# Optimization experiments

Hardware: AMD Instinct MI355X
Metric: run time of the kernel (lower is better)

Reference implementation:

```python
import jax, jax.numpy as jnp
import numpy as np

B, D = 16384, 4096
H1, H2 = 64, 32
EPS_BN = 1e-5


def _lin(k, fi, fo):
    return 0.02 * jax.random.normal(k, (fi, fo), dtype=jnp.float32)


def setup_inputs() -> dict:
    key = jax.random.key(0)
    ks = jax.random.split(key, 8)
    x = jax.random.uniform(ks[0], (B, D), dtype=jnp.float32)
    return {
        "x": x,
        "W_in": _lin(ks[1], D, H1), "b_in": jnp.zeros((H1,), jnp.float32),
        "g1": jnp.ones((H1,), jnp.float32), "bt1": jnp.zeros((H1,), jnp.float32),
        "W_enc": _lin(ks[2], H1, H2), "b_enc": jnp.zeros((H2,), jnp.float32),
        "g2": jnp.ones((H2,), jnp.float32), "bt2": jnp.zeros((H2,), jnp.float32),
        "W_dec": _lin(ks[3], H2, H1), "b_dec": jnp.zeros((H1,), jnp.float32),
        "g3": jnp.ones((H1,), jnp.float32), "bt3": jnp.zeros((H1,), jnp.float32),
        "W_pi": _lin(ks[4], H1, D), "b_pi": jnp.zeros((D,), jnp.float32),
        "W_m": _lin(ks[5], H1, D), "b_m": jnp.zeros((D,), jnp.float32),
        "W_th": _lin(ks[6], H1, D), "b_th": jnp.zeros((D,), jnp.float32),
    }


def preprocess_data(data):
    # torch: s = data.sum(1); s /= median(s); norm = inverse(diag(s)) @ data + 1
    # inverse(diag(s)) @ data is exactly a per-row division by s.
    s = jnp.sum(data, axis=1)
    n = s.shape[0]
    med = jnp.sort(s)[(n - 1) // 2]  # torch.median = lower median
    s = s / med
    norm = jnp.log(data / s[:, None] + 1.0)
    # torch .std() is unbiased (ddof=1)
    return (norm - norm.mean()) / norm.std(ddof=1)


def batchnorm(h, gamma, beta):
    # training-mode BatchNorm1d: biased batch variance, eps=1e-5
    mu = h.mean(axis=0)
    var = h.var(axis=0)
    return (h - mu) * jax.lax.rsqrt(var + EPS_BN) * gamma + beta


def reference(x, W_in, b_in, g1, bt1, W_enc, b_enc, g2, bt2,
              W_dec, b_dec, g3, bt3, W_pi, b_pi, W_m, b_m, W_th, b_th):
    h = preprocess_data(x)
    h = jax.nn.relu(batchnorm(h @ W_in + b_in, g1, bt1))
    h = jax.nn.relu(batchnorm(h @ W_enc + b_enc, g2, bt2))
    h = jax.nn.relu(batchnorm(h @ W_dec + b_dec, g3, bt3))
    PI = jax.nn.sigmoid(h @ W_pi + b_pi)
    M = jnp.exp(h @ W_m + b_m)
    THETA = jnp.exp(h @ W_th + b_th)
    return (PI, M, THETA)
```

## Files before the change

### kernel.cpp

```cpp
#include <hip/hip_runtime.h>

#define BATCH 16384
#define DIM   4096

typedef __bf16 bf16x8 __attribute__((ext_vector_type(8)));
typedef float  f32x4  __attribute__((ext_vector_type(4)));
typedef unsigned short u16x8 __attribute__((ext_vector_type(8)));
typedef unsigned short u16x4 __attribute__((ext_vector_type(4)));

#define BAR_LGKM() asm volatile("s_waitcnt lgkmcnt(0)\ns_barrier" ::: "memory")

#define WS_ROWSUM 0
#define WS_MED    16384
#define WS_NPART  16400
#define WS_SC3    17536
#define WS_CC3    17600
#define WS_A2PART 18432
#define WS_A3PART 34816
#define WS_CPART  67584
#define WS_R      133120
#define WS_A2     1181696
#define WS_A3     1705984
#define WS_WTIN   2754560
#define WS_WTO    2885632

__device__ __forceinline__ unsigned short f2bf(float f){
  union { float f; unsigned u; } v; v.f = f;
  unsigned r = v.u + 0x7FFFu + ((v.u >> 16) & 1u);
  return (unsigned short)(r >> 16);
}

__global__ __launch_bounds__(256) void k_prep_rowsum(
    const float* __restrict__ x, const float* __restrict__ Win,
    const float* __restrict__ Wpi, const float* __restrict__ Wm,
    const float* __restrict__ Wth, float* __restrict__ ws){
  int b = blockIdx.x, t = threadIdx.x;
  if (b < 256) {
    __shared__ unsigned short tile[64][72];
    if (b < 64) {
      int k0 = b * 64;
      int n = t & 63, kb = t >> 6;
      #pragma unroll
      for (int i = 0; i < 16; ++i) {
        int kk = kb * 16 + i;
        tile[n][kk] = f2bf(Win[(size_t)(k0 + kk) * 64 + n]);
      }
      __syncthreads();
      unsigned short* wtin = (unsigned short*)(ws + WS_WTIN);
      int c = t & 7;
      #pragma unroll
      for (int p = 0; p < 2; ++p) {
        int nn = (t >> 3) + p * 32;
        u16x8 v = *(const u16x8*)&tile[nn][c * 8];
        *(u16x8*)(wtin + (size_t)nn * 4096 + k0 + c * 8) = v;
      }
    } else {
      int bm = (b - 64) >> 6;
      int n0 = ((b - 64) & 63) * 64;
      const float* W = (bm == 0) ? Wpi : ((bm == 1) ? Wm : Wth);
      int nn = t & 63, kb = t >> 6;
      #pragma unroll
      for (int i = 0; i < 16; ++i) {
        int k = kb * 16 + i;
        tile[nn][k] = f2bf(W[(size_t)k * 4096 + n0 + nn]);
      }
      __syncthreads();
      unsigned short* wto = (unsigned short*)(ws + WS_WTO);
      int c = t & 7;
      #pragma unroll
      for (int p = 0; p < 2; ++p) {
        int nn2 = (t >> 3) + p * 32;
        u16x8 v = *(const u16x8*)&tile[nn2][c * 8];
        *(u16x8*)(wto + (size_t)bm * 262144 + (size_t)(n0 + nn2) * 64 + c * 8) = v;
      }
    }
  } else {
    int w = t >> 6, lane = t & 63;
    int row = (b - 256) * 4 + w;
    const float4* xr = (const float4*)(x + (size_t)row * DIM);
    float s = 0.f;
    #pragma unroll
    for (int i = 0; i < 16; ++i) {
      float4 v = xr[lane + 64 * i];
      s += (v.x + v.y) + (v.z + v.w);
    }
    #pragma unroll
    for (int m = 32; m; m >>= 1) s += __shfl_xor(s, m);
    if (lane == 0) ws[WS_ROWSUM + row] = s;
  }
}

__global__ __launch_bounds__(1024) void k_median(float* __restrict__ ws){
  __shared__ unsigned keys[16384];
  __shared__ int hist[4096];
  __shared__ int scanbuf[1024];
  __shared__ int selBin, selRank;
  int t = threadIdx.x, lane = t & 63;

  for (int i = t; i < 16384; i += 1024) keys[i] = __float_as_uint(ws[WS_ROWSUM + i]);
  for (int i = t; i < 4096; i += 1024) hist[i] = 0;
  __syncthreads();

  auto scanFind = [&](int target) {
    int s = hist[4*t] + hist[4*t+1] + hist[4*t+2] + hist[4*t+3];
    scanbuf[t] = s;
    __syncthreads();
    for (int off = 1; off < 1024; off <<= 1) {
      int v = scanbuf[t];
      int a = (t >= off) ? scanbuf[t - off] : 0;
      __syncthreads();
      scanbuf[t] = v + a;
      __syncthreads();
    }
    int acc = scanbuf[t] - s;
    #pragma unroll
    for (int j = 0; j < 4; ++j) {
      int c = hist[4*t + j];
      if (acc <= target && target < acc + c) { selBin = 4*t + j; selRank = target - acc; }
      acc += c;
    }
    __syncthreads();
  };

  for (int i = t; i < 16384; i += 1024) {
    unsigned key = keys[i] >> 20;
    unsigned long long unclaimed = __ballot(1);
    int cnt = 0; bool leader = false;
    while (true) {
      int src = (int)(__ffsll((unsigned long long)unclaimed)) - 1;
      unsigned k0 = (unsigned)__shfl((int)key, src);
      unsigned long long eq = __ballot(k0 == key);
      if (k0 == key) { leader = (lane == src); cnt = (int)__popcll(eq); break; }
      unclaimed &= ~eq;
    }
    if (leader) atomicAdd(&hist[key], cnt);
  }
  __syncthreads();
  scanFind(8191);
  unsigned B1 = (unsigned)selBin; int r1 = selRank;
  __syncthreads();
  for (int i = t; i < 4096; i += 1024) hist[i] = 0;
  __syncthreads();
  for (int i = t; i < 16384; i += 1024) {
    unsigned u = keys[i];
    if ((u >> 20) == B1) atomicAdd(&hist[(u >> 8) & 0xFFF], 1);
  }
  __syncthreads();
  scanFind(r1);
  unsigned B2 = (unsigned)selBin; int r2 = selRank;
  __syncthreads();
  for (int i = t; i < 4096; i += 1024) hist[i] = 0;
  __syncthreads();
  unsigned hi24 = (B1 << 12) | B2;
  for (int i = t; i < 16384; i += 1024) {
    unsigned u = keys[i];
    if ((u >> 8) == hi24) atomicAdd(&hist[u & 0xFF], 1);
  }
  __syncthreads();
  scanFind(r2);
  if (t == 0) {
    unsigned bits = (B1 << 20) | (B2 << 8) | (unsigned)selBin;
    ws[WS_MED] = __uint_as_float(bits);
  }
}

__global__ __launch_bounds__(512) void k_passB(const float* __restrict__ x, float* __restrict__ ws){
  __shared__ __align__(16) char Ab[2 * 4096];
  __shared__ __align__(16) char Bb[2 * 8192];
  __shared__ float ainv_s[32];
  __shared__ float redn[8][2];
  __shared__ float cpart[2][64], cqpart[2][64];

  const unsigned short* wtin = (const unsigned short*)(ws + WS_WTIN);
  int tid = threadIdx.x;
  int r0 = (511 - (int)blockIdx.x) * 32;
  float med = ws[WS_MED];
  if (tid < 32) ainv_s[tid] = med / ws[WS_ROWSUM + r0 + tid];
  __syncthreads();

  int w = tid >> 6, lane = tid & 63;
  int li = lane & 15, u = lane >> 4;
  int wrb = (w & 1) * 16;
  int wc  = (w >> 1) * 16;

  int xrow = tid >> 4;
  int xcol0 = (tid & 15) * 4;
  int wn = tid >> 3, wkc = tid & 7;
  float ainv = ainv_s[xrow];

  f32x4 acc = (f32x4){0.f, 0.f, 0.f, 0.f};
  float nsum = 0.f, nsq = 0.f;
  float4 xa0, xa1, xa2, xa3; u16x8 wv0, wv1, wv2, wv3;

  auto LOADT = [&](int tt, float4& xv, u16x8& wq){
    int coff = tt * 64;
    xv = *(const float4*)(x + (size_t)(r0 + xrow) * DIM + coff + xcol0);
    wq = *(const u16x8*)(wtin + (size_t)wn * DIM + coff + wkc * 8);
  };
  auto WRITET = [&](int buf, const float4& xv, const u16x8& wq){
    float n0 = __logf(fmaf(xv.x, ainv, 1.f));
    float n1 = __logf(fmaf(xv.y, ainv, 1.f));
    float n2 = __logf(fmaf(xv.z, ainv, 1.f));
    float n3 = __logf(fmaf(xv.w, ainv, 1.f));
    nsum += (n0 + n1) + (n2 + n3);
    nsq  += (n0*n0 + n1*n1) + (n2*n2 + n3*n3);
    u16x4 p = { f2bf(n0), f2bf(n1), f2bf(n2), f2bf(n3) };
    int c = xcol0 >> 3, sub = (xcol0 >> 2) & 1;
    *(u16x4*)(Ab + buf * 4096 + xrow * 128 + ((c ^ (xrow & 7)) << 4) + sub * 8) = p;
    *(u16x8*)(Bb + buf * 8192 + wn * 128 + ((wkc ^ (wn & 7)) << 4)) = wq;
  };
  int arow = wrb + li, brow = wc + li;
  auto DOMFMA = [&](int p){
    const char* Au = Ab + p * 4096;
    const char* Bu = Bb + p * 8192;
    #pragma unroll
    for (int kk = 0; kk < 2; ++kk) {
      bf16x8 aF = *(const bf16x8*)(Au + arow * 128 + (((kk * 4 + u) ^ (arow & 7)) << 4));
      bf16x8 bF = *(const bf16x8*)(Bu + brow * 128 + (((kk * 4 + u) ^ (brow & 7)) << 4));
      acc = __builtin_amdgcn_mfma_f32_16x16x32_bf16(bF, aF, acc, 0, 0, 0);
    }
  };

  LOADT(0, xa0, wv0);
  LOADT(1, xa1, wv1);
  LOADT(2, xa2, wv2);
  WRITET(0, xa0, wv0);
  BAR_LGKM();
  for (int t = 0; t < 64; t += 4) {
    if (t + 3 < 64) LOADT(t + 3, xa3, wv3);
    WRITET(1, xa1, wv1);
    DOMFMA(0);
    BAR_LGKM();
    if (t + 4 < 64) LOADT(t + 4, xa0, wv0);
    WRITET(0, xa2, wv2);
    DOMFMA(1);
    BAR_LGKM();
    if (t + 5 < 64) LOADT(t + 5, xa1, wv1);
    if (t + 3 < 64) WRITET(1, xa3, wv3);
    DOMFMA(0);
    BAR_LGKM();
    if (t + 6 < 64) LOADT(t + 6, xa2, wv2);
    if (t + 4 < 64) WRITET(0, xa0, wv0);
    DOMFMA(1);
    BAR_LGKM();
  }

  float* R = ws + WS_R;
  *(f32x4*)(R + (size_t)(r0 + wrb + li) * 64 + wc + u * 4) = acc;

  float s0 = acc[0], s1 = acc[1], s2 = acc[2], s3 = acc[3];
  float q0 = acc[0]*acc[0], q1 = acc[1]*acc[1], q2 = acc[2]*acc[2], q3 = acc[3]*acc[3];
  #pragma unroll
  for (int m = 1; m < 16; m <<= 1) {
    s0 += __shfl_xor(s0, m); s1 += __shfl_xor(s1, m);
    s2 += __shfl_xor(s2, m); s3 += __shfl_xor(s3, m);
    q0 += __shfl_xor(q0, m); q1 += __shfl_xor(q1, m);
    q2 += __shfl_xor(q2, m); q3 += __shfl_xor(q3, m);
  }
  if (li == 0) {
    int cb = wc + u * 4;
    cpart[w & 1][cb + 0] = s0; cpart[w & 1][cb + 1] = s1;
    cpart[w & 1][cb + 2] = s2; cpart[w & 1][cb + 3] = s3;
    cqpart[w & 1][cb + 0] = q0; cqpart[w & 1][cb + 1] = q1;
    cqpart[w & 1][cb + 2] = q2; cqpart[w & 1][cb + 3] = q3;
  }
  #pragma unroll
  for (int m = 32; m; m >>= 1) { nsum += __shfl_xor(nsum, m); nsq += __shfl_xor(nsq, m); }
  if (lane == 0) { redn[w][0] = nsum; redn[w][1] = nsq; }
  BAR_LGKM();
  if (tid < 64) {
    ws[WS_CPART + blockIdx.x * 128 + tid]      = cpart[0][tid] + cpart[1][tid];
    ws[WS_CPART + blockIdx.x * 128 + 64 + tid] = cqpart[0][tid] + cqpart[1][tid];
  }
  if (tid == 0) {
    float S = 0.f, Q = 0.f;
    for (int i = 0; i < 8; ++i) { S += redn[i][0]; Q += redn[i][1]; }
    ws[WS_NPART + blockIdx.x * 2]     = S;
    ws[WS_NPART + blockIdx.x * 2 + 1] = Q;
  }
}

__global__ __launch_bounds__(256) void k_layer1(const float* __restrict__ g1, const float* __restrict__ bt1,
                         const float* __restrict__ Wenc, const float* __restrict__ benc,
                         float* __restrict__ ws){
  __shared__ float sc1[64], cc1[64];
  __shared__ float h1[64][65];
  __shared__ float we[64][33];
  __shared__ float sred[4][64], qred[4][64];
  __shared__ float sigred[4][2];
  __shared__ float sig2s;
  int t = threadIdx.x, lane = t & 63, w4 = t >> 6;

  {
    float s = 0.f, q = 0.f;
    for (int b = t; b < 512; b += 256) { s += ws[WS_NPART + b * 2]; q += ws[WS_NPART + b * 2 + 1]; }
    #pragma unroll
    for (int m = 32; m; m >>= 1) { s += __shfl_xor(s, m); q += __shfl_xor(q, m); }
    if (lane == 0) { sigred[w4][0] = s; sigred[w4][1] = q; }
  }
  {
    int col = t & 63, grp = t >> 6;
    float S = 0.f, Q = 0.f;
    for (int b = grp * 128; b < grp * 128 + 128; ++b) {
      S += ws[WS_CPART + b * 128 + col];
      Q += ws[WS_CPART + b * 128 + 64 + col];
    }
    sred[grp][col] = S; qred[grp][col] = Q;
  }
  for (int i = t; i < 2048; i += 256) we[i >> 5][i & 31] = Wenc[i];
  __syncthreads();
  if (t == 0) {
    double Sn = (double)sigred[0][0] + sigred[1][0] + sigred[2][0] + sigred[3][0];
    double Qn = (double)sigred[0][1] + sigred[1][1] + sigred[2][1] + sigred[3][1];
    double N = 67108864.0;
    sig2s = (float)((Qn - Sn * Sn / N) / (N - 1.0));
  }
  __syncthreads();
  if (t < 64) {
    float Sc = sred[0][t] + sred[1][t] + sred[2][t] + sred[3][t];
    float Qc = qred[0][t] + qred[1][t] + qred[2][t] + qred[3][t];
    float cm = Sc * (1.f / 16384.f);
    float cv = Qc * (1.f / 16384.f) - cm * cm;
    float sc = g1[t] * rsqrtf(cv + sig2s * 1e-5f);
    sc1[t] = sc; cc1[t] = bt1[t] - cm * sc;
  }
  __syncthreads();

  int r0 = blockIdx.x * 64;
  const float* R = ws + WS_R;
  for (int i = t; i < 4096; i += 256) {
    int row = i >> 6, col = i & 63;
    float v = fmaf(R[(size_t)(r0 + row) * 64 + col], sc1[col], cc1[col]);
    h1[row][col] = fmaxf(v, 0.f);
  }
  __syncthreads();
  int row = t & 63, cb = t >> 6;
  float a[8];
  #pragma unroll
  for (int j = 0; j < 8; ++j) a[j] = benc[cb * 8 + j];
  for (int k = 0; k < 64; ++k) {
    float hv = h1[row][k];
    #pragma unroll
    for (int j = 0; j < 8; ++j) a[j] = fmaf(hv, we[k][cb * 8 + j], a[j]);
  }
  float* A2 = ws + WS_A2;
  #pragma unroll
  for (int j = 0; j < 8; ++j) A2[(size_t)(r0 + row) * 32 + cb * 8 + j] = a[j];
  #pragma unroll
  for (int j = 0; j < 8; ++j) {
    float s = a[j], q = a[j] * a[j];
    #pragma unroll
    for (int m = 32; m; m >>= 1) { s += __shfl_xor(s, m); q += __shfl_xor(q, m); }
    if (lane == 0) {
      int c = cb * 8 + j;
      ws[WS_A2PART + blockIdx.x * 64 + c * 2]     = s;
      ws[WS_A2PART + blockIdx.x * 64 + c * 2 + 1] = q;
    }
  }
}

__global__ __launch_bounds__(256) void k_layer2(const float* __restrict__ g2, const float* __restrict__ bt2,
                         const float* __restrict__ Wdec, const float* __restrict__ bdec,
                         float* __restrict__ ws){
  __shared__ float h2[64][33];
  __shared__ float wd[32][65];
  __shared__ float sc2[32], cc2[32];
  __shared__ float sred2[8][32], qred2[8][32];
  int t = threadIdx.x, lane = t & 63;
  {
    int col = t & 31, grp = t >> 5;
    float S = 0.f, Q = 0.f;
    for (int b = grp * 32; b < grp * 32 + 32; ++b) {
      S += ws[WS_A2PART + b * 64 + col * 2];
      Q += ws[WS_A2PART + b * 64 + col * 2 + 1];
    }
    sred2[grp][col] = S; qred2[grp][col] = Q;
  }
  for (int i = t; i < 2048; i += 256) wd[i >> 6][i & 63] = Wdec[i];
  __syncthreads();
  if (t < 32) {
    float Sc = 0.f, Qc = 0.f;
    #pragma unroll
    for (int g = 0; g < 8; ++g) { Sc += sred2[g][t]; Qc += qred2[g][t]; }
    float cm = Sc * (1.f / 16384.f);
    float cv = Qc * (1.f / 16384.f) - cm * cm;
    float sc = g2[t] * rsqrtf(cv + 1e-5f);
    sc2[t] = sc; cc2[t] = bt2[t] - cm * sc;
  }
  __syncthreads();
  int r0 = blockIdx.x * 64;
  const float* A2 = ws + WS_A2;
  for (int i = t; i < 2048; i += 256) {
    int row = i >> 5, col = i & 31;
    float v = fmaf(A2[(size_t)(r0 + row) * 32 + col], sc2[col], cc2[col]);
    h2[row][col] = fmaxf(v, 0.f);
  }
  __syncthreads();
  int row = t & 63, cb = t >> 6;
  float a[16];
  #pragma unroll
  for (int j = 0; j < 16; ++j) a[j] = bdec[cb * 16 + j];
  for (int k = 0; k < 32; ++k) {
    float hv = h2[row][k];
    #pragma unroll
    for (int j = 0; j < 16; ++j) a[j] = fmaf(hv, wd[k][cb * 16 + j], a[j]);
  }
  float* A3 = ws + WS_A3;
  #pragma unroll
  for (int j = 0; j < 16; ++j) A3[(size_t)(r0 + row) * 64 + cb * 16 + j] = a[j];
  #pragma unroll
  for (int j = 0; j < 16; ++j) {
    float s = a[j], q = a[j] * a[j];
    #pragma unroll
    for (int m = 32; m; m >>= 1) { s += __shfl_xor(s, m); q += __shfl_xor(q, m); }
    if (lane == 0) {
      int c = cb * 16 + j;
      ws[WS_A3PART + blockIdx.x * 128 + c * 2]     = s;
      ws[WS_A3PART + blockIdx.x * 128 + c * 2 + 1] = q;
    }
  }
}

__global__ void k_red3(const float* __restrict__ g3, const float* __restrict__ bt3, float* __restrict__ ws){
  __shared__ float red[128];
  int t = threadIdx.x;
  if (t < 128) {
    float s = 0.f;
    for (int b = 0; b < 256; ++b) s += ws[WS_A3PART + b * 128 + t];
    red[t] = s;
  }
  __syncthreads();
  if (t < 64) {
    float S = red[2 * t], Q = red[2 * t + 1];
    float cm = S * (1.f / 16384.f);
    float cv = Q * (1.f / 16384.f) - cm * cm;
    float sc = g3[t] * rsqrtf(cv + 1e-5f);
    ws[WS_SC3 + t] = sc; ws[WS_CC3 + t] = bt3[t] - cm * sc;
  }
}

__global__ __launch_bounds__(512) void k_out(const float* __restrict__ bpi, const float* __restrict__ bm,
                      const float* __restrict__ bth, float* __restrict__ out,
                      float* __restrict__ ws){
  __shared__ __align__(16) char WB[256 * 128];
  int t = threadIdx.x;
  int bx = blockIdx.x;
  int rb = bx >> 4, cb = bx & 15;
  int r0 = rb * 128, c0 = cb * 256;
  int w = t >> 6, lane = t & 63;
  int u = lane >> 4, li = lane & 15;

  const float* A3 = ws + WS_A3;
  const float* SC = ws + WS_SC3;
  const float* CC = ws + WS_CC3;
  int arow = r0 + w * 16 + li;
  const float4* a3p = (const float4*)(A3 + (size_t)arow * 64);
  bf16x8 aF[2];
  #pragma unroll
  for (int h = 0; h < 2; ++h) {
    float4 v0 = a3p[h * 8 + u * 2];
    float4 v1 = a3p[h * 8 + u * 2 + 1];
    int kb = h * 32 + u * 8;
    u16x8 uu;
    uu[0] = f2bf(fmaxf(fmaf(v0.x, SC[kb+0], CC[kb+0]), 0.f));
    uu[1] = f2bf(fmaxf(fmaf(v0.y, SC[kb+1], CC[kb+1]), 0.f));
    uu[2] = f2bf(fmaxf(fmaf(v0.z, SC[kb+2], CC[kb+2]), 0.f));
    uu[3] = f2bf(fmaxf(fmaf(v0.w, SC[kb+3], CC[kb+3]), 0.f));
    uu[4] = f2bf(fmaxf(fmaf(v1.x, SC[kb+4], CC[kb+4]), 0.f));
    uu[5] = f2bf(fmaxf(fmaf(v1.y, SC[kb+5], CC[kb+5]), 0.f));
    uu[6] = f2bf(fmaxf(fmaf(v1.z, SC[kb+6], CC[kb+6]), 0.f));
    uu[7] = f2bf(fmaxf(fmaf(v1.w, SC[kb+7], CC[kb+7]), 0.f));
    aF[h] = __builtin_bit_cast(bf16x8, uu);
  }

  const unsigned short* wto = (const unsigned short*)(ws + WS_WTO);
  for (int m = 0; m < 3; ++m) {
    BAR_LGKM();
    const unsigned short* src = wto + (size_t)m * 262144 + (size_t)c0 * 64;
    for (int ch = t; ch < 2048; ch += 512) {
      int n = ch >> 3, kc = ch & 7;
      u16x8 vchunk = *(const u16x8*)(src + n * 64 + kc * 8);
      *(u16x8*)(WB + n * 128 + ((kc ^ (n & 7)) << 4)) = vchunk;
    }
    BAR_LGKM();
    const float* bias = (m == 0) ? bpi : ((m == 1) ? bm : bth);
    float* po = out + (size_t)m * 67108864;
    for (int cg = 0; cg < 16; ++cg) {
      int n = cg * 16 + li;
      bf16x8 bF0 = *(const bf16x8*)(WB + n * 128 + (((0 + u) ^ (n & 7)) << 4));
      bf16x8 bF1 = *(const bf16x8*)(WB + n * 128 + (((4 + u) ^ (n & 7)) << 4));
      f32x4 d = (f32x4){0.f, 0.f, 0.f, 0.f};
      d = __builtin_amdgcn_mfma_f32_16x16x32_bf16(bF0, aF[0], d, 0, 0, 0);
      d = __builtin_amdgcn_mfma_f32_16x16x32_bf16(bF1, aF[1], d, 0, 0, 0);
      int colb = c0 + cg * 16 + u * 4;
      f32x4 bv = *(const f32x4*)(bias + colb);
      f32x4 z;
      #pragma unroll
      for (int r = 0; r < 4; ++r) {
        float zz = d[r] + bv[r];
        z[r] = (m == 0) ? (1.f / (1.f + __expf(-zz))) : __expf(zz);
      }
      *(f32x4*)(po + (size_t)arow * 4096 + colb) = z;
    }
  }
}

extern "C" void kernel_launch(void* const* d_in, const int* in_sizes, int n_in,
                              void* d_out, int out_size, void* d_ws, size_t ws_size,
                              hipStream_t stream) {
  const float* x    = (const float*)d_in[0];
  const float* Win  = (const float*)d_in[1];
  const float* g1   = (const float*)d_in[3];
  const float* bt1  = (const float*)d_in[4];
  const float* Wenc = (const float*)d_in[5];
  const float* benc = (const float*)d_in[6];
  const float* g2   = (const float*)d_in[7];
  const float* bt2  = (const float*)d_in[8];
  const float* Wdec = (const float*)d_in[9];
  const float* bdec = (const float*)d_in[10];
  const float* g3   = (const float*)d_in[11];
  const float* bt3  = (const float*)d_in[12];
  const float* Wpi  = (const float*)d_in[13];
  const float* bpi  = (const float*)d_in[14];
  const float* Wm   = (const float*)d_in[15];
  const float* bm   = (const float*)d_in[16];
  const float* Wth  = (const float*)d_in[17];
  const float* bth  = (const float*)d_in[18];
  float* ws  = (float*)d_ws;
  float* out = (float*)d_out;

  hipLaunchKernelGGL(k_prep_rowsum, dim3(4352), dim3(256),  0, stream, x, Win, Wpi, Wm, Wth, ws);
  hipLaunchKernelGGL(k_median,      dim3(1),    dim3(1024), 0, stream, ws);
  hipLaunchKernelGGL(k_passB,       dim3(512),  dim3(512),  0, stream, x, ws);
  hipLaunchKernelGGL(k_layer1,      dim3(256),  dim3(256),  0, stream, g1, bt1, Wenc, benc, ws);
  hipLaunchKernelGGL(k_layer2,      dim3(256),  dim3(256),  0, stream, g2, bt2, Wdec, bdec, ws);
  hipLaunchKernelGGL(k_red3,        dim3(1),    dim3(256),  0, stream, g3, bt3, ws);
  hipLaunchKernelGGL(k_out,         dim3(2048), dim3(512),  0, stream, bpi, bm, bth, out, ws);
}
```

Before: 413.5 us.

## Make k_out persistent with register-resident weights and prefetched activation rows

The output kernel now launches 256 blocks, each covering 1024 rows by 256 columns, instead of 2048 blocks of 128 rows. The output-weight fragments are loaded straight from global memory into registers and reused across eight row tiles, which removes the LDS staging and the two barriers per output head. Activation rows for the next tile are prefetched while the current tile is processed. Fewer blocks on a large GPU can lower parallelism and memory-level concurrency for this store-bound kernel, and the register arrays raise register pressure.

```diff
diff --git a/kernel.cpp b/kernel.cpp
--- a/kernel.cpp
+++ b/kernel.cpp
@@ -442,65 +442,89 @@
 __global__ __launch_bounds__(512) void k_out(const float* __restrict__ bpi, const float* __restrict__ bm,
                       const float* __restrict__ bth, float* __restrict__ out,
                       float* __restrict__ ws){
-  __shared__ __align__(16) char WB[256 * 128];
   int t = threadIdx.x;
   int bx = blockIdx.x;
-  int rb = bx >> 4, cb = bx & 15;
-  int r0 = rb * 128, c0 = cb * 256;
+  int rs = bx >> 4, cb = bx & 15;
+  int r0 = rs * 1024, c0 = cb * 256;
   int w = t >> 6, lane = t & 63;
   int u = lane >> 4, li = lane & 15;
 
   const float* A3 = ws + WS_A3;
   const float* SC = ws + WS_SC3;
   const float* CC = ws + WS_CC3;
-  int arow = r0 + w * 16 + li;
-  const float4* a3p = (const float4*)(A3 + (size_t)arow * 64);
-  bf16x8 aF[2];
-  #pragma unroll
-  for (int h = 0; h < 2; ++h) {
-    float4 v0 = a3p[h * 8 + u * 2];
-    float4 v1 = a3p[h * 8 + u * 2 + 1];
-    int kb = h * 32 + u * 8;
-    u16x8 uu;
-    uu[0] = f2bf(fmaxf(fmaf(v0.x, SC[kb+0], CC[kb+0]), 0.f));
-    uu[1] = f2bf(fmaxf(fmaf(v0.y, SC[kb+1], CC[kb+1]), 0.f));
-    uu[2] = f2bf(fmaxf(fmaf(v0.z, SC[kb+2], CC[kb+2]), 0.f));
-    uu[3] = f2bf(fmaxf(fmaf(v0.w, SC[kb+3], CC[kb+3]), 0.f));
-    uu[4] = f2bf(fmaxf(fmaf(v1.x, SC[kb+4], CC[kb+4]), 0.f));
-    uu[5] = f2bf(fmaxf(fmaf(v1.y, SC[kb+5], CC[kb+5]), 0.f));
-    uu[6] = f2bf(fmaxf(fmaf(v1.z, SC[kb+6], CC[kb+6]), 0.f));
-    uu[7] = f2bf(fmaxf(fmaf(v1.w, SC[kb+7], CC[kb+7]), 0.f));
-    aF[h] = __builtin_bit_cast(bf16x8, uu);
-  }
-
+  float4 sA0 = *(const float4*)(SC + u * 8);
+  float4 sA1 = *(const float4*)(SC + u * 8 + 4);
+  float4 sB0 = *(const float4*)(SC + 32 + u * 8);
+  float4 sB1 = *(const float4*)(SC + 32 + u * 8 + 4);
+  float4 cA0 = *(const float4*)(CC + u * 8);
+  float4 cA1 = *(const float4*)(CC + u * 8 + 4);
+  float4 cB0 = *(const float4*)(CC + 32 + u * 8);
+  float4 cB1 = *(const float4*)(CC + 32 + u * 8 + 4);
+
+  int rowbase = r0 + w * 128 + li;
   const unsigned short* wto = (const unsigned short*)(ws + WS_WTO);
+
   for (int m = 0; m < 3; ++m) {
-    BAR_LGKM();
     const unsigned short* src = wto + (size_t)m * 262144 + (size_t)c0 * 64;
-    for (int ch = t; ch < 2048; ch += 512) {
-      int n = ch >> 3, kc = ch & 7;
-      u16x8 vchunk = *(const u16x8*)(src + n * 64 + kc * 8);
-      *(u16x8*)(WB + n * 128 + ((kc ^ (n & 7)) << 4)) = vchunk;
-    }
-    BAR_LGKM();
     const float* bias = (m == 0) ? bpi : ((m == 1) ? bm : bth);
     float* po = out + (size_t)m * 67108864;
-    for (int cg = 0; cg < 16; ++cg) {
-      int n = cg * 16 + li;
-      bf16x8 bF0 = *(const bf16x8*)(WB + n * 128 + (((0 + u) ^ (n & 7)) << 4));
-      bf16x8 bF1 = *(const bf16x8*)(WB + n * 128 + (((4 + u) ^ (n & 7)) << 4));
-      f32x4 d = (f32x4){0.f, 0.f, 0.f, 0.f};
-      d = __builtin_amdgcn_mfma_f32_16x16x32_bf16(bF0, aF[0], d, 0, 0, 0);
-      d = __builtin_amdgcn_mfma_f32_16x16x32_bf16(bF1, aF[1], d, 0, 0, 0);
-      int colb = c0 + cg * 16 + u * 4;
-      f32x4 bv = *(const f32x4*)(bias + colb);
-      f32x4 z;
+    #pragma unroll
+    for (int half = 0; half < 2; ++half) {
+      bf16x8 bF0[8], bF1[8];
       #pragma unroll
-      for (int r = 0; r < 4; ++r) {
-        float zz = d[r] + bv[r];
-        z[r] = (m == 0) ? (1.f / (1.f + __expf(-zz))) : __expf(zz);
-      }
-      *(f32x4*)(po + (size_t)arow * 4096 + colb) = z;
+      for (int cg = 0; cg < 8; ++cg) {
+        int n = (half * 8 + cg) * 16 + li;
+        bF0[cg] = *(const bf16x8*)(src + (size_t)n * 64 + u * 8);
+        bF1[cg] = *(const bf16x8*)(src + (size_t)n * 64 + 32 + u * 8);
+      }
+      float4 p0, p1, p2, p3;
+      {
+        const float4* a3p = (const float4*)(A3 + (size_t)rowbase * 64);
+        p0 = a3p[u * 2]; p1 = a3p[u * 2 + 1]; p2 = a3p[8 + u * 2]; p3 = a3p[8 + u * 2 + 1];
+      }
+      for (int tile = 0; tile < 8; ++tile) {
+        float4 n0, n1, n2, n3;
+        if (tile < 7) {
+          const float4* a3p = (const float4*)(A3 + (size_t)(rowbase + (tile + 1) * 16) * 64);
+          n0 = a3p[u * 2]; n1 = a3p[u * 2 + 1]; n2 = a3p[8 + u * 2]; n3 = a3p[8 + u * 2 + 1];
+        }
+        u16x8 uu0, uu1;
+        uu0[0] = f2bf(fmaxf(fmaf(p0.x, sA0.x, cA0.x), 0.f));
+        uu0[1] = f2bf(fmaxf(fmaf(p0.y, sA0.y, cA0.y), 0.f));
+        uu0[2] = f2bf(fmaxf(fmaf(p0.z, sA0.z, cA0.z), 0.f));
+        uu0[3] = f2bf(fmaxf(fmaf(p0.w, sA0.w, cA0.w), 0.f));
+        uu0[4] = f2bf(fmaxf(fmaf(p1.x, sA1.x, cA1.x), 0.f));
+        uu0[5] = f2bf(fmaxf(fmaf(p1.y, sA1.y, cA1.y), 0.f));
+        uu0[6] = f2bf(fmaxf(fmaf(p1.z, sA1.z, cA1.z), 0.f));
+        uu0[7] = f2bf(fmaxf(fmaf(p1.w, sA1.w, cA1.w), 0.f));
+        uu1[0] = f2bf(fmaxf(fmaf(p2.x, sB0.x, cB0.x), 0.f));
+        uu1[1] = f2bf(fmaxf(fmaf(p2.y, sB0.y, cB0.y), 0.f));
+        uu1[2] = f2bf(fmaxf(fmaf(p2.z, sB0.z, cB0.z), 0.f));
+        uu1[3] = f2bf(fmaxf(fmaf(p2.w, sB0.w, cB0.w), 0.f));
+        uu1[4] = f2bf(fmaxf(fmaf(p3.x, sB1.x, cB1.x), 0.f));
+        uu1[5] = f2bf(fmaxf(fmaf(p3.y, sB1.y, cB1.y), 0.f));
+        uu1[6] = f2bf(fmaxf(fmaf(p3.z, sB1.z, cB1.z), 0.f));
+        uu1[7] = f2bf(fmaxf(fmaf(p3.w, sB1.w, cB1.w), 0.f));
+        bf16x8 aF0 = __builtin_bit_cast(bf16x8, uu0);
+        bf16x8 aF1 = __builtin_bit_cast(bf16x8, uu1);
+        int arow = rowbase + tile * 16;
+        #pragma unroll
+        for (int cg = 0; cg < 8; ++cg) {
+          f32x4 d = (f32x4){0.f, 0.f, 0.f, 0.f};
+          d = __builtin_amdgcn_mfma_f32_16x16x32_bf16(bF0[cg], aF0, d, 0, 0, 0);
+          d = __builtin_amdgcn_mfma_f32_16x16x32_bf16(bF1[cg], aF1, d, 0, 0, 0);
+          int colb = c0 + (half * 8 + cg) * 16 + u * 4;
+          f32x4 bv = *(const f32x4*)(bias + colb);
+          f32x4 z;
+          #pragma unroll
+          for (int r = 0; r < 4; ++r) {
+            float zz = d[r] + bv[r];
+            z[r] = (m == 0) ? (1.f / (1.f + __expf(-zz))) : __expf(zz);
+          }
+          *(f32x4*)(po + (size_t)arow * 4096 + colb) = z;
+        }
+        p0 = n0; p1 = n1; p2 = n2; p3 = n3;
+      }
     }
   }
 }
@@ -535,5 +559,5 @@
   hipLaunchKernelGGL(k_layer1,      dim3(256),  dim3(256),  0, stream, g1, bt1, Wenc, benc, ws);
   hipLaunchKernelGGL(k_layer2,      dim3(256),  dim3(256),  0, stream, g2, bt2, Wdec, bdec, ws);
   hipLaunchKernelGGL(k_red3,        dim3(1),    dim3(256),  0, stream, g3, bt3, ws);
-  hipLaunchKernelGGL(k_out,         dim3(2048), dim3(512),  0, stream, bpi, bm, bth, out, ws);
-}
+  hipLaunchKernelGGL(k_out,         dim3(256),  dim3(512),  0, stream, bpi, bm, bth, out, ws);
+}
```

New measurement: 377.0 us (median of 2 runs). 1.1x faster.
